# Kernel optimization log

Measured on AMD Instinct MI355X. Metric: run time of the kernel, lower is better.

Reference implementation:

```python
import jax, jax.numpy as jnp
import numpy as np

TOPK = 10
NUM_CLASSES = 80
ALPHA = 0.5
BETA = 6.0
EPS = 1e-9
IOU_EPS = 1e-7


def _make_anchors(img=640, strides=(8, 16, 32)):
    pts = []
    for s in strides:
        n = img // s
        ax = (np.arange(n, dtype=np.float32) + 0.5) * s
        gy, gx = np.meshgrid(ax, ax, indexing='ij')
        pts.append(np.stack([gx.ravel(), gy.ravel()], axis=-1))
    return jnp.asarray(np.concatenate(pts, axis=0), dtype=jnp.float32)  # [8400, 2]


def setup_inputs() -> dict:
    key = jax.random.key(0)
    ks = jax.random.split(key, 8)
    bs, ng, nc = 32, 64, NUM_CLASSES
    anc_points = _make_anchors()
    na = anc_points.shape[0]  # 8400
    pd_scores = jax.random.uniform(ks[0], (bs, na, nc), dtype=jnp.float32)
    pwh = jax.random.uniform(ks[1], (bs, na, 2), minval=10.0, maxval=100.0)
    pxy = anc_points[None] + jax.random.normal(ks[2], (bs, na, 2)) * 8.0
    pd_bboxes = jnp.concatenate([pxy - pwh / 2, pxy + pwh / 2], axis=-1)
    gxy = jax.random.uniform(ks[3], (bs, ng, 2), minval=50.0, maxval=590.0)
    gwh = jax.random.uniform(ks[4], (bs, ng, 2), minval=20.0, maxval=200.0)
    gt_bboxes = jnp.clip(jnp.concatenate([gxy - gwh / 2, gxy + gwh / 2], axis=-1), 0.0, 640.0)
    gt_labels = jax.random.randint(ks[5], (bs, ng, 1), 0, nc)
    num_gt = jax.random.randint(ks[6], (bs,), 1, ng + 1)
    mask_gt = (jnp.arange(ng)[None, :] < num_gt[:, None])[..., None]  # bool [bs, ng, 1]
    return {"pd_scores": pd_scores, "pd_bboxes": pd_bboxes, "anc_points": anc_points,
            "gt_labels": gt_labels, "gt_bboxes": gt_bboxes, "mask_gt": mask_gt}


def _iou_xyxy(b1, b2):
    # b1: [bs, na, 1, 4], b2: [bs, 1, ng, 4] -> [bs, na, ng]
    inter_w = jnp.maximum(jnp.minimum(b1[..., 2], b2[..., 2]) - jnp.maximum(b1[..., 0], b2[..., 0]), 0.0)
    inter_h = jnp.maximum(jnp.minimum(b1[..., 3], b2[..., 3]) - jnp.maximum(b1[..., 1], b2[..., 1]), 0.0)
    inter = inter_w * inter_h
    a1 = (b1[..., 2] - b1[..., 0]) * (b1[..., 3] - b1[..., 1])
    a2 = (b2[..., 2] - b2[..., 0]) * (b2[..., 3] - b2[..., 1])
    return inter / (a1 + a2 - inter + IOU_EPS)


def _assign(pd_scores, pd_bboxes, anc_points, gt_labels, gt_bboxes, mask_gt):
    bs, na, nc = pd_scores.shape
    ng = gt_bboxes.shape[1]
    dt = pd_scores.dtype

    # --- candidates whose center lies strictly inside the GT box ---
    lt = gt_bboxes[:, None, :, :2]          # [bs,1,ng,2]
    rb = gt_bboxes[:, None, :, 2:]
    xy = anc_points[None, :, None, :]       # [1,na,1,2]
    deltas = jnp.concatenate([xy - lt, rb - xy], axis=-1)  # [bs,na,ng,4]
    mask_in_gts = deltas.min(axis=-1) > EPS                 # [bs,na,ng]
    valid = mask_gt[..., 0].astype(bool)                    # [bs,ng]
    mask = mask_in_gts & valid[:, None, :]

    # --- alignment metric = score[label]^alpha * iou^beta, zeroed outside mask ---
    labels = gt_labels[..., 0].astype(jnp.int32)            # [bs,ng]
    idx = jnp.broadcast_to(labels[:, None, :], (bs, na, ng))
    gathered = jnp.take_along_axis(pd_scores, idx, axis=2)  # [bs,na,ng]
    bbox_scores = jnp.where(mask, gathered, 0.0)
    overlaps = jnp.where(mask, _iou_xyxy(pd_bboxes[:, :, None, :], gt_bboxes[:, None, :, :]), 0.0)
    safe_scores = jnp.where(mask, gathered, 1.0)  # avoids 0**0.5 grad issues; masked out below
    align_metric = jnp.where(mask, safe_scores ** ALPHA * overlaps ** BETA, 0.0)

    # --- top-k anchors per GT (over anchor dim) ---
    k = min(TOPK, na)
    _, topk_idx = jax.lax.top_k(jnp.swapaxes(align_metric, 1, 2), k)  # [bs,ng,k]
    bidx = jnp.arange(bs)[:, None, None]
    gidx = jnp.arange(ng)[None, :, None]
    in_topk = jnp.zeros((bs, ng, na), dtype=bool).at[bidx, gidx, topk_idx].set(True)
    in_topk = jnp.swapaxes(in_topk, 1, 2) & valid[:, None, :]  # [bs,na,ng]
    mask_pos = (in_topk & mask).astype(dt)

    # --- resolve anchors assigned to multiple GTs by highest IoU ---
    multi = mask_pos.sum(-1, keepdims=True) > 1
    is_max = jax.nn.one_hot(jnp.argmax(overlaps, axis=-1), ng, dtype=dt)
    mask_pos = jnp.where(multi, is_max, mask_pos)
    fg_mask = mask_pos.sum(-1) > 0                  # [bs,na] bool
    target_gt_idx = jnp.argmax(mask_pos, axis=-1)   # [bs,na]

    # --- gather targets ---
    flat_idx = target_gt_idx + jnp.arange(bs)[:, None] * ng
    target_labels = jnp.maximum(gt_labels[..., 0].reshape(-1)[flat_idx], 0)  # [bs,na]
    target_bboxes = gt_bboxes.reshape(-1, 4)[flat_idx]                       # [bs,na,4]
    one_hot = jax.nn.one_hot(target_labels, nc, dtype=dt) * fg_mask[..., None].astype(dt)

    fgf = fg_mask[..., None].astype(dt)
    norm_align = jnp.maximum((align_metric * fgf).max(-1, keepdims=True), EPS)
    norm_overlap = jnp.maximum((overlaps * fgf).max(-1, keepdims=True), EPS)
    t_scores = ((align_metric / norm_align) * (overlaps / norm_overlap) * fgf).max(-1)  # [bs,na]
    target_scores = one_hot * t_scores[..., None]
    return target_labels, target_bboxes, target_scores, fg_mask, target_gt_idx


def reference(pd_scores, pd_bboxes, anc_points, gt_labels, gt_bboxes, mask_gt):
    return _assign(pd_scores, pd_bboxes, anc_points, gt_labels, gt_bboxes, mask_gt)
```

## Files before the change

kernel.cpp:

```cpp
#include <hip/hip_runtime.h>
#include <math.h>

#define NC 80
#define TOPKK 10
#define EPSF 1e-9f
#define IOU_EPSF 1e-7f
#define NA 8400
#define NGMAX 64

typedef float f4nt __attribute__((ext_vector_type(4)));

__device__ __forceinline__ float iou_xyxy(float px0, float py0, float px1, float py1,
                                          float parea,
                                          float gx0, float gy0, float gx1, float gy1,
                                          float garea) {
    float iw = fmaxf(fminf(px1, gx1) - fmaxf(px0, gx0), 0.0f);
    float ih = fmaxf(fminf(py1, gy1) - fmaxf(py0, gy0), 0.0f);
    float inter = iw * ih;
    return inter / (parea + garea - inter + IOU_EPSF);
}

__device__ __forceinline__ float align_metric(float s, float ov) {
    float ov2 = ov * ov;
    return sqrtf(s) * (ov2 * ov2 * ov2);
}

__global__ __launch_bounds__(256) void topk_rect_kernel(
    const float* __restrict__ pd_scores, const float* __restrict__ pd_bboxes,
    const int* __restrict__ gt_labels, const float* __restrict__ gt_bboxes,
    const int* __restrict__ mask_gt,
    int* __restrict__ idx_out, int ng, int total_bg)
{
    int lin = blockIdx.x * 4 + (threadIdx.x >> 6);
    if (lin >= total_bg) return;
    int b = lin / ng;
    int g = lin - b * ng;
    int lane = threadIdx.x & 63;
    int* __restrict__ slot = idx_out + (long)lin * TOPKK;

    if (mask_gt[b * ng + g] == 0) {
        if (lane < TOPKK) slot[lane] = -1;
        return;
    }

    int lab = gt_labels[b * ng + g];
    float4 gb = ((const float4*)gt_bboxes)[b * ng + g];
    float garea = (gb.z - gb.x) * (gb.w - gb.y);
    const float* __restrict__ srow = pd_scores + ((long)b * NA) * NC + lab;
    const float4* __restrict__ pbb = (const float4*)(pd_bboxes + (long)b * NA * 4);

    const int ls[3] = {8, 16, 32};
    const int ln[3] = {80, 40, 20};
    const int lb[3] = {0, 6400, 8000};
    int jlo[3], ilo[3], rw[3], cnt[3];
    int tot = 0;
#pragma unroll
    for (int l = 0; l < 3; ++l) {
        float s = (float)ls[l];
        int j0 = (int)floorf(gb.x / s - 0.5f) - 1; if (j0 < 0) j0 = 0;
        int j1 = (int)ceilf (gb.z / s - 0.5f) + 1; if (j1 > ln[l] - 1) j1 = ln[l] - 1;
        int i0 = (int)floorf(gb.y / s - 0.5f) - 1; if (i0 < 0) i0 = 0;
        int i1 = (int)ceilf (gb.w / s - 0.5f) + 1; if (i1 > ln[l] - 1) i1 = ln[l] - 1;
        int w = j1 - j0 + 1; if (w < 0) w = 0;
        int h = i1 - i0 + 1; if (h < 0) h = 0;
        jlo[l] = j0; ilo[l] = i0; rw[l] = w; cnt[l] = w * h; tot += cnt[l];
    }

    float lv[TOPKK]; int li[TOPKK];
#pragma unroll
    for (int j = 0; j < TOPKK; ++j) { lv[j] = -1.0f; li[j] = -1; }

    for (int t = lane; t < tot; t += 64) {
        int l = 0, r = t;
        if (r >= cnt[0]) { r -= cnt[0]; l = 1; }
        if (l == 1 && r >= cnt[1]) { r -= cnt[1]; l = 2; }
        int i  = r / rw[l];
        int j  = r - i * rw[l];
        int ii = ilo[l] + i, jj = jlo[l] + j;
        int a  = lb[l] + ii * ln[l] + jj;
        float s  = (float)ls[l];
        float ax = (jj + 0.5f) * s, ay = (ii + 0.5f) * s;
        float d0 = ax - gb.x, d1 = ay - gb.y, d2 = gb.z - ax, d3 = gb.w - ay;
        float dmin = fminf(fminf(d0, d1), fminf(d2, d3));
        if (dmin > EPSF) {
            float4 pb = pbb[a];
            float parea = (pb.z - pb.x) * (pb.w - pb.y);
            float ov = iou_xyxy(pb.x, pb.y, pb.z, pb.w, parea,
                                gb.x, gb.y, gb.z, gb.w, garea);
            float sc = srow[(long)a * NC];
            float v = align_metric(sc, ov);
            if (v > 0.0f && v > lv[TOPKK - 1]) {
                float nv[TOPKK]; int ni[TOPKK];
#pragma unroll
                for (int q = 0; q < TOPKK; ++q) {
                    bool keep = (lv[q] >= v);
                    bool atp  = (q == 0) ? !keep : (!keep && (lv[q - 1] >= v));
                    nv[q] = keep ? lv[q] : (atp ? v : lv[q - 1]);
                    ni[q] = keep ? li[q] : (atp ? a : li[q - 1]);
                }
#pragma unroll
                for (int q = 0; q < TOPKK; ++q) { lv[q] = nv[q]; li[q] = ni[q]; }
            }
        }
    }

    int m = 0;
    for (int it = 0; it < TOPKK; ++it) {
        unsigned long long myk = (lv[0] > 0.0f)
            ? (((unsigned long long)__float_as_uint(lv[0]) << 32)
               | (unsigned)(~(unsigned)li[0]))
            : 0ull;
        unsigned long long k = myk;
#pragma unroll
        for (int off = 32; off > 0; off >>= 1) {
            unsigned long long o = __shfl_xor(k, off, 64);
            k = (o > k) ? o : k;
        }
        if (k == 0ull) break;
        if (myk == k) {
            slot[it] = li[0];
#pragma unroll
            for (int q = 0; q < TOPKK - 1; ++q) { lv[q] = lv[q + 1]; li[q] = li[q + 1]; }
            lv[TOPKK - 1] = -1.0f; li[TOPKK - 1] = -1;
        }
        m++;
    }

    if (m < TOPKK && lane == 0) {
        int p = m;
        for (int a = 0; p < TOPKK && a < NA; ++a) {
            int l  = (a < 6400) ? 0 : ((a < 8000) ? 1 : 2);
            int rr = a - lb[l];
            int ii = rr / ln[l];
            int jj = rr - ii * ln[l];
            float s  = (float)ls[l];
            float ax = (jj + 0.5f) * s, ay = (ii + 0.5f) * s;
            float d0 = ax - gb.x, d1 = ay - gb.y, d2 = gb.z - ax, d3 = gb.w - ay;
            float dmin = fminf(fminf(d0, d1), fminf(d2, d3));
            bool positive = false;
            if (dmin > EPSF) {
                float4 pb = pbb[a];
                float parea = (pb.z - pb.x) * (pb.w - pb.y);
                float ov = iou_xyxy(pb.x, pb.y, pb.z, pb.w, parea,
                                    gb.x, gb.y, gb.z, gb.w, garea);
                float sc = srow[(long)a * NC];
                positive = (align_metric(sc, ov) > 0.0f);
            }
            if (!positive) slot[p++] = a;
        }
    }
}

__global__ __launch_bounds__(256) void assign_scores_kernel(
    const float* __restrict__ pd_scores, const float* __restrict__ pd_bboxes,
    const float* __restrict__ anc, const int* __restrict__ gt_labels,
    const float* __restrict__ gt_bboxes, const int* __restrict__ mask_gt,
    const int* __restrict__ idx_in,
    float* __restrict__ out_labels, float* __restrict__ out_bboxes,
    float* __restrict__ out_scores, float* __restrict__ out_fg,
    float* __restrict__ out_tgt, int ng, int blocksPerB)
{
    __shared__ float4 sgt[NGMAX];
    __shared__ float  sarea[NGMAX];
    __shared__ int    slab[NGMAX];
    __shared__ int    svalid[NGMAX];
    __shared__ unsigned long long smask[256];
    __shared__ int    plab[256];
    __shared__ float  pt[256];

    int b  = blockIdx.x / blocksPerB;
    int a0 = (blockIdx.x - b * blocksPerB) * 256;
    int a  = a0 + threadIdx.x;

    smask[threadIdx.x] = 0ull;
    for (int g = threadIdx.x; g < ng; g += 256) {
        float4 gb = ((const float4*)gt_bboxes)[b * ng + g];
        sgt[g] = gb;
        sarea[g] = (gb.z - gb.x) * (gb.w - gb.y);
        slab[g] = gt_labels[b * ng + g];
        svalid[g] = mask_gt[b * ng + g];
    }
    __syncthreads();

    {
        int nent = ng * TOPKK;
        const int* lst = idx_in + (long)b * nent;
        for (int i = threadIdx.x; i < nent; i += 256) {
            int aa = lst[i];
            unsigned off = (unsigned)(aa - a0);
            if (aa >= 0 && off < 256u) {
                atomicOr(&smask[off], 1ull << (i / TOPKK));
            }
        }
    }
    __syncthreads();

    bool alive = (a < NA);
    int labi0 = slab[0] < 0 ? 0 : slab[0];
    int labi = labi0; float t = 0.0f;

    if (alive) {
        long ba = (long)b * NA + a;
        unsigned long long w = smask[threadIdx.x];
        if (w == 0ull) {
            out_labels[ba] = (float)labi0;
            ((float4*)out_bboxes)[ba] = sgt[0];
            out_fg[ba]  = 0.0f;
            out_tgt[ba] = 0.0f;
        } else {
            float ax = anc[a * 2 + 0];
            float ay = anc[a * 2 + 1];
            float4 pb = ((const float4*)pd_bboxes)[ba];
            float parea = (pb.z - pb.x) * (pb.w - pb.y);
            const float* __restrict__ srow = pd_scores + ba * NC;

            int cnt = 0, pos_g = 0;
            float best_ov = 0.0f; int best_g = 0;
            float m_align = 0.0f, m_ov = 0.0f, t_raw = 0.0f;

            for (int g = 0; g < ng; ++g) {
                if (svalid[g] == 0) break;
                float4 gb = sgt[g];
                float d0 = ax - gb.x, d1 = ay - gb.y, d2 = gb.z - ax, d3 = gb.w - ay;
                float dmin = fminf(fminf(d0, d1), fminf(d2, d3));
                bool mask = (dmin > EPSF);
                float ov = 0.0f, al = 0.0f;
                if (mask) {
                    ov = iou_xyxy(pb.x, pb.y, pb.z, pb.w, parea,
                                  gb.x, gb.y, gb.z, gb.w, sarea[g]);
                    float s = srow[slab[g]];
                    al = align_metric(s, ov);
                }
                bool pos = mask && ((w >> g) & 1ull);
                if (pos) { if (cnt == 0) pos_g = g; cnt++; }
                if (ov > best_ov) { best_ov = ov; best_g = g; }
                m_align = fmaxf(m_align, al);
                m_ov    = fmaxf(m_ov, ov);
                t_raw   = fmaxf(t_raw, al * ov);
            }

            int fg  = (cnt > 0) ? 1 : 0;
            int tgt = (cnt > 1) ? best_g : ((cnt == 1) ? pos_g : 0);

            labi = slab[tgt]; if (labi < 0) labi = 0;
            out_labels[ba] = (float)labi;
            ((float4*)out_bboxes)[ba] = sgt[tgt];
            out_fg[ba]  = (float)fg;
            out_tgt[ba] = (float)tgt;

            if (fg) {
                float na_ = fmaxf(m_align, EPSF);
                float no_ = fmaxf(m_ov, EPSF);
                t = (t_raw / na_) / no_;
            }
        }
    }

    plab[threadIdx.x] = labi;
    pt[threadIdx.x]   = t;
    __syncthreads();

    int cnt_rows = NA - a0; if (cnt_rows > 256) cnt_rows = 256;
    int tot4 = cnt_rows * (NC / 4);
    f4nt* __restrict__ oslab = (f4nt*)(out_scores + ((long)b * NA + a0) * NC);
    for (int i = threadIdx.x; i < tot4; i += 256) {
        int al = i / (NC / 4);
        int cg = (i - al * (NC / 4)) * 4;
        int lab = plab[al];
        float tv = pt[al];
        f4nt o;
        o.x = (cg     == lab) ? tv : 0.0f;
        o.y = (cg + 1 == lab) ? tv : 0.0f;
        o.z = (cg + 2 == lab) ? tv : 0.0f;
        o.w = (cg + 3 == lab) ? tv : 0.0f;
        __builtin_nontemporal_store(o, &oslab[i]);
    }
}

extern "C" void kernel_launch(void* const* d_in, const int* in_sizes, int n_in,
                              void* d_out, int out_size, void* d_ws, size_t ws_size,
                              hipStream_t stream) {
    const float* pd_scores = (const float*)d_in[0];
    const float* pd_bboxes = (const float*)d_in[1];
    const float* anc       = (const float*)d_in[2];
    const int*   gt_labels = (const int*)d_in[3];
    const float* gt_bboxes = (const float*)d_in[4];
    const int*   mask_gt   = (const int*)d_in[5];

    int na = in_sizes[2] / 2;
    int bs = in_sizes[0] / (na * NC);
    int ng = in_sizes[3] / bs;

    long nBA = (long)bs * na;
    float* out        = (float*)d_out;
    float* out_labels = out;
    float* out_bboxes = out + nBA;
    float* out_scores = out + nBA * 5;
    float* out_fg     = out + nBA * 85;
    float* out_tgt    = out + nBA * 86;

    int* idx = (int*)d_ws;

    int total_bg = bs * ng;
    int nblk = (total_bg + 3) / 4;
    topk_rect_kernel<<<nblk, 256, 0, stream>>>(
        pd_scores, pd_bboxes, gt_labels, gt_bboxes, mask_gt, idx, ng, total_bg);

    int bpb = (na + 255) / 256;
    assign_scores_kernel<<<bs * bpb, 256, 0, stream>>>(
        pd_scores, pd_bboxes, anc, gt_labels, gt_bboxes, mask_gt, idx,
        out_labels, out_bboxes, out_scores, out_fg, out_tgt, ng, bpb);
}
```

Measured before the change: 196.3 us.

## Software-pipeline top-k candidate loads and cull GTs per anchor block

In the top-k kernel, the loads of the candidate's box and score are issued one iteration ahead of the IoU and insertion work, and the integer division is replaced by a float-reciprocal divide with a correction step. In the assign kernel, each block keeps only the valid GT boxes whose y-range overlaps the anchor rows it covers, compacted with a ballot, so the per-anchor loop visits fewer GTs. Output stores become nontemporal. The aim is to hide load latency and cut redundant per-anchor GT work. The cost is extra index remapping and registers, and the GT-order tie-breaking must still match the reference.

```diff
diff --git a/kernel.cpp b/kernel.cpp
--- a/kernel.cpp
+++ b/kernel.cpp
@@ -24,6 +24,27 @@
     float ov2 = ov * ov;
     return sqrtf(s) * (ov2 * ov2 * ov2);
 }
+
+#define TK_INSERT(vv, aa) do {                                              \
+    float nv[TOPKK]; int ni[TOPKK];                                         \
+    _Pragma("unroll")                                                       \
+    for (int q = 0; q < TOPKK; ++q) {                                       \
+        bool keep = (lv[q] >= (vv));                                        \
+        bool atp  = (q == 0) ? !keep : (!keep && (lv[q - 1] >= (vv)));      \
+        nv[q] = keep ? lv[q] : (atp ? (vv) : lv[q - 1]);                    \
+        ni[q] = keep ? li[q] : (atp ? (aa) : li[q - 1]);                    \
+    }                                                                       \
+    _Pragma("unroll")                                                       \
+    for (int q = 0; q < TOPKK; ++q) { lv[q] = nv[q]; li[q] = ni[q]; }       \
+} while (0)
+
+#define TK_PROCESS() do {                                                   \
+    float parea_ = (pb_p.z - pb_p.x) * (pb_p.w - pb_p.y);                   \
+    float ov_ = iou_xyxy(pb_p.x, pb_p.y, pb_p.z, pb_p.w, parea_,            \
+                         gb.x, gb.y, gb.z, gb.w, garea);                    \
+    float v_ = align_metric(sc_p, ov_);                                     \
+    if (v_ > 0.0f && v_ > lv[TOPKK - 1]) TK_INSERT(v_, a_p);                \
+} while (0)
 
 __global__ __launch_bounds__(256) void topk_rect_kernel(
     const float* __restrict__ pd_scores, const float* __restrict__ pd_bboxes,
@@ -53,6 +74,7 @@
     const int ln[3] = {80, 40, 20};
     const int lb[3] = {0, 6400, 8000};
     int jlo[3], ilo[3], rw[3], cnt[3];
+    float inv_rw[3];
     int tot = 0;
 #pragma unroll
     for (int l = 0; l < 3; ++l) {
@@ -64,45 +86,39 @@
         int w = j1 - j0 + 1; if (w < 0) w = 0;
         int h = i1 - i0 + 1; if (h < 0) h = 0;
         jlo[l] = j0; ilo[l] = i0; rw[l] = w; cnt[l] = w * h; tot += cnt[l];
+        inv_rw[l] = (w > 0) ? 1.0f / (float)w : 0.0f;
     }
 
     float lv[TOPKK]; int li[TOPKK];
 #pragma unroll
     for (int j = 0; j < TOPKK; ++j) { lv[j] = -1.0f; li[j] = -1; }
 
+    int a_p = 0; bool ok_p = false; float sc_p = 0.0f;
+    float4 pb_p = make_float4(0.f, 0.f, 0.f, 0.f);
     for (int t = lane; t < tot; t += 64) {
         int l = 0, r = t;
         if (r >= cnt[0]) { r -= cnt[0]; l = 1; }
         if (l == 1 && r >= cnt[1]) { r -= cnt[1]; l = 2; }
-        int i  = r / rw[l];
-        int j  = r - i * rw[l];
+        int i = (int)((float)r * inv_rw[l]);
+        int j = r - i * rw[l];
+        if (j < 0) { --i; j += rw[l]; }
+        else if (j >= rw[l]) { ++i; j -= rw[l]; }
         int ii = ilo[l] + i, jj = jlo[l] + j;
         int a  = lb[l] + ii * ln[l] + jj;
         float s  = (float)ls[l];
         float ax = (jj + 0.5f) * s, ay = (ii + 0.5f) * s;
         float d0 = ax - gb.x, d1 = ay - gb.y, d2 = gb.z - ax, d3 = gb.w - ay;
         float dmin = fminf(fminf(d0, d1), fminf(d2, d3));
-        if (dmin > EPSF) {
-            float4 pb = pbb[a];
-            float parea = (pb.z - pb.x) * (pb.w - pb.y);
-            float ov = iou_xyxy(pb.x, pb.y, pb.z, pb.w, parea,
-                                gb.x, gb.y, gb.z, gb.w, garea);
-            float sc = srow[(long)a * NC];
-            float v = align_metric(sc, ov);
-            if (v > 0.0f && v > lv[TOPKK - 1]) {
-                float nv[TOPKK]; int ni[TOPKK];
-#pragma unroll
-                for (int q = 0; q < TOPKK; ++q) {
-                    bool keep = (lv[q] >= v);
-                    bool atp  = (q == 0) ? !keep : (!keep && (lv[q - 1] >= v));
-                    nv[q] = keep ? lv[q] : (atp ? v : lv[q - 1]);
-                    ni[q] = keep ? li[q] : (atp ? a : li[q - 1]);
-                }
-#pragma unroll
-                for (int q = 0; q < TOPKK; ++q) { lv[q] = nv[q]; li[q] = ni[q]; }
-            }
-        }
-    }
+        bool ok = dmin > EPSF;
+        float4 pb = pb_p; float sc = 0.0f;
+        if (ok) {
+            pb = pbb[a];
+            sc = srow[(long)a * NC];
+        }
+        if (ok_p) TK_PROCESS();
+        a_p = a; pb_p = pb; sc_p = sc; ok_p = ok;
+    }
+    if (ok_p) TK_PROCESS();
 
     int m = 0;
     for (int it = 0; it < TOPKK; ++it) {
@@ -163,7 +179,10 @@
     __shared__ float4 sgt[NGMAX];
     __shared__ float  sarea[NGMAX];
     __shared__ int    slab[NGMAX];
-    __shared__ int    svalid[NGMAX];
+    __shared__ int    sgi[NGMAX];
+    __shared__ int    snf;
+    __shared__ float4 sgt0;
+    __shared__ int    slab0s;
     __shared__ unsigned long long smask[256];
     __shared__ int    plab[256];
     __shared__ float  pt[256];
@@ -173,12 +192,49 @@
     int a  = a0 + threadIdx.x;
 
     smask[threadIdx.x] = 0ull;
-    for (int g = threadIdx.x; g < ng; g += 256) {
-        float4 gb = ((const float4*)gt_bboxes)[b * ng + g];
-        sgt[g] = gb;
-        sarea[g] = (gb.z - gb.x) * (gb.w - gb.y);
-        slab[g] = gt_labels[b * ng + g];
-        svalid[g] = mask_gt[b * ng + g];
+
+    const int Lb[3] = {0, 6400, 8000};
+    const int Lc[3] = {6400, 1600, 400};
+    const int Ln[3] = {80, 40, 20};
+    const int Ls[3] = {8, 16, 32};
+    float ymin = 1e30f, ymax = -1e30f;
+    {
+        int aend = a0 + 255; if (aend > NA - 1) aend = NA - 1;
+#pragma unroll
+        for (int l = 0; l < 3; ++l) {
+            int as_ = a0   > Lb[l]             ? a0   : Lb[l];
+            int ae_ = aend < Lb[l] + Lc[l] - 1 ? aend : Lb[l] + Lc[l] - 1;
+            if (as_ <= ae_) {
+                int r0 = (as_ - Lb[l]) / Ln[l];
+                int r1 = (ae_ - Lb[l]) / Ln[l];
+                float s = (float)Ls[l];
+                ymin = fminf(ymin, (r0 + 0.5f) * s);
+                ymax = fmaxf(ymax, (r1 + 0.5f) * s);
+            }
+        }
+    }
+
+    if (threadIdx.x < 64) {
+        int g = threadIdx.x;
+        bool ok = false;
+        float4 gb = make_float4(0.f, 0.f, 0.f, 0.f);
+        if (g < ng && mask_gt[b * ng + g] != 0) {
+            gb = ((const float4*)gt_bboxes)[b * ng + g];
+            ok = (gb.y < ymax) && (gb.w > ymin);
+        }
+        unsigned long long bal = __ballot(ok);
+        int pos = __popcll(bal & ((1ull << g) - 1ull));
+        if (ok) {
+            sgt[pos]   = gb;
+            sarea[pos] = (gb.z - gb.x) * (gb.w - gb.y);
+            slab[pos]  = gt_labels[b * ng + g];
+            sgi[pos]   = g;
+        }
+        if (g == 0) {
+            snf    = __popcll(bal);
+            sgt0   = ((const float4*)gt_bboxes)[b * ng];
+            slab0s = gt_labels[b * ng];
+        }
     }
     __syncthreads();
 
@@ -196,17 +252,18 @@
     __syncthreads();
 
     bool alive = (a < NA);
-    int labi0 = slab[0] < 0 ? 0 : slab[0];
+    int labi0 = slab0s < 0 ? 0 : slab0s;
     int labi = labi0; float t = 0.0f;
 
     if (alive) {
         long ba = (long)b * NA + a;
         unsigned long long w = smask[threadIdx.x];
         if (w == 0ull) {
-            out_labels[ba] = (float)labi0;
-            ((float4*)out_bboxes)[ba] = sgt[0];
-            out_fg[ba]  = 0.0f;
-            out_tgt[ba] = 0.0f;
+            __builtin_nontemporal_store((float)labi0, &out_labels[ba]);
+            f4nt g0; g0.x = sgt0.x; g0.y = sgt0.y; g0.z = sgt0.z; g0.w = sgt0.w;
+            __builtin_nontemporal_store(g0, &((f4nt*)out_bboxes)[ba]);
+            __builtin_nontemporal_store(0.0f, &out_fg[ba]);
+            __builtin_nontemporal_store(0.0f, &out_tgt[ba]);
         } else {
             float ax = anc[a * 2 + 0];
             float ay = anc[a * 2 + 1];
@@ -214,41 +271,47 @@
             float parea = (pb.z - pb.x) * (pb.w - pb.y);
             const float* __restrict__ srow = pd_scores + ba * NC;
 
-            int cnt = 0, pos_g = 0;
-            float best_ov = 0.0f; int best_g = 0;
+            int cnt = 0, pos_k = 0, best_k = 0;
+            float best_ov = 0.0f;
             float m_align = 0.0f, m_ov = 0.0f, t_raw = 0.0f;
-
-            for (int g = 0; g < ng; ++g) {
-                if (svalid[g] == 0) break;
-                float4 gb = sgt[g];
-                float d0 = ax - gb.x, d1 = ay - gb.y, d2 = gb.z - ax, d3 = gb.w - ay;
+            int nf = snf;
+
+            for (int k = 0; k < nf; ++k) {
+                float4 gbk = sgt[k];
+                float d0 = ax - gbk.x, d1 = ay - gbk.y;
+                float d2 = gbk.z - ax, d3 = gbk.w - ay;
                 float dmin = fminf(fminf(d0, d1), fminf(d2, d3));
                 bool mask = (dmin > EPSF);
                 float ov = 0.0f, al = 0.0f;
                 if (mask) {
                     ov = iou_xyxy(pb.x, pb.y, pb.z, pb.w, parea,
-                                  gb.x, gb.y, gb.z, gb.w, sarea[g]);
-                    float s = srow[slab[g]];
-                    al = align_metric(s, ov);
+                                  gbk.x, gbk.y, gbk.z, gbk.w, sarea[k]);
+                    float sc = srow[slab[k]];
+                    al = align_metric(sc, ov);
                 }
-                bool pos = mask && ((w >> g) & 1ull);
-                if (pos) { if (cnt == 0) pos_g = g; cnt++; }
-                if (ov > best_ov) { best_ov = ov; best_g = g; }
+                bool pos = mask && ((w >> sgi[k]) & 1ull);
+                if (pos) { if (cnt == 0) pos_k = k; cnt++; }
+                if (ov > best_ov) { best_ov = ov; best_k = k; }
                 m_align = fmaxf(m_align, al);
                 m_ov    = fmaxf(m_ov, ov);
                 t_raw   = fmaxf(t_raw, al * ov);
             }
 
-            int fg  = (cnt > 0) ? 1 : 0;
-            int tgt = (cnt > 1) ? best_g : ((cnt == 1) ? pos_g : 0);
-
-            labi = slab[tgt]; if (labi < 0) labi = 0;
-            out_labels[ba] = (float)labi;
-            ((float4*)out_bboxes)[ba] = sgt[tgt];
-            out_fg[ba]  = (float)fg;
-            out_tgt[ba] = (float)tgt;
-
-            if (fg) {
+            if (cnt == 0) {
+                __builtin_nontemporal_store((float)labi0, &out_labels[ba]);
+                f4nt g0; g0.x = sgt0.x; g0.y = sgt0.y; g0.z = sgt0.z; g0.w = sgt0.w;
+                __builtin_nontemporal_store(g0, &((f4nt*)out_bboxes)[ba]);
+                __builtin_nontemporal_store(0.0f, &out_fg[ba]);
+                __builtin_nontemporal_store(0.0f, &out_tgt[ba]);
+            } else {
+                int tk = (cnt > 1) ? best_k : pos_k;
+                labi = slab[tk]; if (labi < 0) labi = 0;
+                __builtin_nontemporal_store((float)labi, &out_labels[ba]);
+                float4 tb = sgt[tk];
+                f4nt tb4; tb4.x = tb.x; tb4.y = tb.y; tb4.z = tb.z; tb4.w = tb.w;
+                __builtin_nontemporal_store(tb4, &((f4nt*)out_bboxes)[ba]);
+                __builtin_nontemporal_store(1.0f, &out_fg[ba]);
+                __builtin_nontemporal_store((float)sgi[tk], &out_tgt[ba]);
                 float na_ = fmaxf(m_align, EPSF);
                 float no_ = fmaxf(m_ov, EPSF);
                 t = (t_raw / na_) / no_;
```

Result: no change. 193.3 us (-1.6%).
